# Kernel tuning notes

Measured on AMD Instinct MI355X. Metric: run time of the kernel, lower is better.

## Reference

```python
import jax, jax.numpy as jnp
import numpy as np

NLAT, NLON = 361, 720
LMAX = NLAT               # equiangular grid: lmax = nlat
MMAX = NLON // 2 + 1      # mmax = nlon//2 + 1
B, C = 1, 128


def _precompute_legpoly(mmax, lmax, t, csphase=True):
    """Associated Legendre vandermonde P_l^m(cos t), orthonormal, inverse=True
    (norm factor 1 for 'ortho'). Shape [mmax, lmax, nlat]. Setup-time numpy only."""
    x = np.cos(t)
    nmax = max(mmax, lmax)
    vdm = np.zeros((nmax, nmax, len(x)))
    vdm[0, 0] = np.sqrt(1.0 / (4.0 * np.pi))
    for l in range(1, nmax):
        vdm[l - 1, l] = np.sqrt(2 * l + 1) * x * vdm[l - 1, l - 1]
        vdm[l, l] = np.sqrt((2 * l + 1) * (1 + x) * (1 - x) / (2 * l)) * vdm[l - 1, l - 1]
    for l in range(2, nmax):
        for m in range(l - 1):
            a = np.sqrt((2 * l - 1) / (l - m) * (2 * l + 1) / (l + m))
            b = np.sqrt((l + m - 1) / (l - m) * (2 * l + 1) / (2 * l - 3) * (l - m - 1) / (l + m))
            vdm[m, l] = a * x * vdm[m, l - 1] - b * vdm[m, l - 2]
    vdm = vdm[:mmax, :lmax]
    if csphase:
        vdm[1::2] *= -1.0  # Condon-Shortley phase on odd m
    return vdm


def setup_inputs() -> dict:
    key = jax.random.key(0)
    # spherical harmonic coefficients as real view: [B, C, lmax, mmax, 2]
    x_real = jax.random.normal(key, (B, C, LMAX, MMAX, 2), dtype=jnp.float32)
    # equiangular (Clenshaw-Curtiss) colatitudes, t = flip(arccos(cos(pi*j/(n-1))))
    t = np.pi * np.arange(NLAT) / (NLAT - 1)
    pct = jnp.asarray(_precompute_legpoly(MMAX, LMAX, t), dtype=jnp.float32)  # [mmax, lmax, nlat]
    return {"x_real": x_real, "pct": pct}


def reference(x_real, pct):
    # single-device case: comm sizes == 1, all distributed transposes are identity
    # and nlatpad == nlonpad == 0.
    # per-m triangular Legendre contraction over l (torch einsum '...lmr,mlk->...kmr')
    xs = jnp.einsum('bclmr,mlk->bckmr', x_real, pct)        # [B, C, nlat, mmax, 2]
    xc = jax.lax.complex(xs[..., 0], xs[..., 1])            # [B, C, nlat, mmax]
    # inverse real FFT along longitude, norm='forward' (no 1/n scaling on inverse)
    out = jnp.fft.irfft(xc, n=NLON, axis=-1, norm='forward')  # [B, C, nlat, nlon]
    return out.astype(x_real.dtype)
```

## Files before the change

kernel.cpp:

```cpp
#include <hip/hip_runtime.h>
#include <cstddef>

#define CC   128
#define LDIM 361
#define MDIM 361
#define KDIM 361
#define NLON 720
#define LP   384
#define KP   384
#define KTP  384
#define MRP  736
#define NP   768
#define CK   (CC*KDIM)
#define CR   (2*CC)

typedef __attribute__((ext_vector_type(8))) short short8;
typedef __attribute__((ext_vector_type(4))) float floatx4;

__device__ __forceinline__ unsigned short f2bf(float f) {
    union { float f; unsigned u; } v; v.f = f;
    unsigned u = v.u;
    u += 0x7fffu + ((u >> 16) & 1u);
    return (unsigned short)(u >> 16);
}

__device__ __forceinline__ void async_copy16(const void* g, void* l) {
    __builtin_amdgcn_global_load_lds(
        (const __attribute__((address_space(1))) void*)g,
        (__attribute__((address_space(3))) void*)l, 16, 0, 0);
}

__device__ __forceinline__ int xcd_swz(int id, int P) {
    int x = id & 7, g = id >> 3;
    int q = P >> 3, r = P & 7;
    int start = (x < r) ? x * (q + 1) : r * (q + 1) + (x - r) * q;
    return start + g;
}

__global__ void sht_gen_T(unsigned short* __restrict__ Tp) {
    int idx = blockIdx.x * 256 + threadIdx.x;
    if (idx >= NP * MRP) return;
    int n = idx / MRP, mr = idx - n * MRP;
    float v = 0.f;
    if (n < NLON && mr < 2 * MDIM) {
        int m = mr >> 1, im = mr & 1;
        if (m == 0)            v = im ? 0.f : 1.f;
        else if (m == MDIM-1)  v = im ? 0.f : ((n & 1) ? -1.f : 1.f);
        else {
            int ph = (m * n) % NLON;
            float ang = (float)ph * (float)(3.14159265358979323846 / 360.0);
            v = im ? (-2.f * sinf(ang)) : (2.f * cosf(ang));
        }
    }
    Tp[idx] = f2bf(v);
}

__global__ __launch_bounds__(256)
void sht_prep_x(const float* __restrict__ x, unsigned short* __restrict__ xA) {
    __shared__ float tp[2][32 * 65 + 4];
    const int mt = blockIdx.x;
    const int lt = blockIdx.y;
    const int c  = blockIdx.z;
    const int t  = threadIdx.x;

    #pragma unroll
    for (int u = 0; u < 8; ++u) {
        int p  = t + 256 * u;
        int li = p >> 5, mi = p & 31;
        int l = lt * 64 + li, m = mt * 32 + mi;
        float2 v = make_float2(0.f, 0.f);
        if (l < LDIM && m < MDIM)
            v = *(const float2*)(x + ((size_t)(c * LDIM + l) * MDIM + m) * 2);
        tp[0][mi * 65 + li] = v.x;
        tp[1][mi * 65 + li] = v.y;
    }
    __syncthreads();

    #pragma unroll
    for (int u = 0; u < 2; ++u) {
        int s  = t + 256 * u;
        int mi = s >> 4, rr = (s >> 3) & 1, lo = (s & 7) * 8;
        int m = mt * 32 + mi;
        if (m >= MDIM) continue;
        const float* pl = &tp[rr][mi * 65];
        short8 h;
        #pragma unroll
        for (int e = 0; e < 8; ++e)
            h[e] = (short)f2bf(pl[lo + e]);
        *(short8*)(xA + ((size_t)m * CR + 2 * c + rr) * LP + lt * 64 + lo) = h;
    }
}

__global__ __launch_bounds__(256)
void sht_prep_pct(const float* __restrict__ pct, unsigned short* __restrict__ pctT) {
    __shared__ float tile[64][65];
    const int m  = blockIdx.y;
    const int bx = blockIdx.x;
    const int kt = bx % 6, lt = bx / 6;
    const int l0 = lt * 64, k0 = kt * 64;
    const int t  = threadIdx.x;

    const int ki = t & 63, lb = t >> 6;
    #pragma unroll
    for (int u = 0; u < 16; ++u) {
        int li = lb + 4 * u;
        int l = l0 + li, k = k0 + ki;
        float v = 0.f;
        if (l < LDIM && k < KDIM)
            v = pct[((size_t)m * LDIM + l) * KDIM + k];
        tile[li][ki] = v;
    }
    __syncthreads();

    #pragma unroll
    for (int u = 0; u < 2; ++u) {
        int s = t + 256 * u;
        int ko = s >> 3, lo = (s & 7) * 8;
        short8 h;
        #pragma unroll
        for (int e = 0; e < 8; ++e)
            h[e] = (short)f2bf(tile[lo + e][ko]);
        *(short8*)(pctT + ((size_t)m * KP + k0 + ko) * LP + l0 + lo) = h;
    }
}

__global__ __launch_bounds__(512)
void sht_stageA6(const unsigned short* __restrict__ pctT, const unsigned short* __restrict__ xA,
                 unsigned short* __restrict__ xsT) {
    __shared__ unsigned short As[3][128 * 32];
    __shared__ unsigned short Bs[3][384 * 32];

    const int p   = xcd_swz(blockIdx.x, 2 * MDIM);
    const int m   = p >> 1, ct = p & 1;
    const int c0  = ct * 128;
    const int t   = threadIdx.x;
    const int w   = t >> 6, L = t & 63;
    const int wr  = w & 1, wc = w >> 1;
    const int lane15 = L & 15, quad = L >> 4;
    const int arr = t >> 2, alq = (t & 3) ^ (arr & 3);

    const unsigned short* xAm = xA + (size_t)m * CR * LP;
    const unsigned short* pTm = pctT + (size_t)m * KP * LP;

    floatx4 acc[4][6] = {};

    auto stage = [&](int buf, int kb) {
        async_copy16(xAm + (size_t)(c0 + arr) * LP + kb + alq * 8,
                     &As[buf][(w * 64) * 8]);
        #pragma unroll
        for (int u = 0; u < 3; ++u) {
            int s = u * 512 + t;
            int rr = s >> 2, lq = (s & 3) ^ (rr & 3);
            async_copy16(pTm + (size_t)rr * LP + kb + lq * 8,
                         &Bs[buf][(u * 512 + w * 64) * 8]);
        }
    };

    const int NT = LP / 32;
    stage(0, 0);
    stage(1, 32);

    for (int it = 0; it < NT; ++it) {
        const int cb = it % 3;
        if (it + 1 < NT) { asm volatile("s_waitcnt vmcnt(4)" ::: "memory"); }
        else             { asm volatile("s_waitcnt vmcnt(0)" ::: "memory"); }
        __builtin_amdgcn_sched_barrier(0);
        __builtin_amdgcn_s_barrier();
        __builtin_amdgcn_sched_barrier(0);

        short8 af[4], bf[6];
        #pragma unroll
        for (int i = 0; i < 4; ++i) {
            int row = wr * 64 + i * 16 + lane15;
            af[i] = *(const short8*)&As[cb][(row * 4 + (quad ^ (row & 3))) * 8];
        }
        #pragma unroll
        for (int j = 0; j < 6; ++j) {
            int row = wc * 96 + j * 16 + lane15;
            bf[j] = *(const short8*)&Bs[cb][(row * 4 + (quad ^ (row & 3))) * 8];
        }
        __builtin_amdgcn_s_setprio(1);
        #pragma unroll
        for (int i = 0; i < 4; ++i)
            #pragma unroll
            for (int j = 0; j < 6; ++j)
                acc[i][j] = __builtin_amdgcn_mfma_f32_16x16x32_bf16(af[i], bf[j], acc[i][j], 0, 0, 0);
        __builtin_amdgcn_s_setprio(0);

        if (it + 2 < NT) stage((it + 2) % 3, (it + 2) * 32);
    }

    #pragma unroll
    for (int i = 0; i < 4; ++i) {
        #pragma unroll
        for (int j = 0; j < 6; ++j) {
            int k = wc * 96 + j * 16 + lane15;
            #pragma unroll
            for (int e = 0; e < 4; ++e) {
                int cr = c0 + wr * 64 + i * 16 + quad * 4 + e;
                xsT[((size_t)m * CR + cr) * KTP + k] = f2bf(acc[i][j][e]);
            }
        }
    }
}

__global__ __launch_bounds__(256)
void sht_xs_tr(const unsigned short* __restrict__ xsT, unsigned short* __restrict__ xs) {
    __shared__ unsigned tile32[64 * 65];
    const int c  = blockIdx.y;
    const int bx = blockIdx.x;
    const int mt = bx / 6, kt = bx % 6;
    const int m0 = mt * 64, k0 = kt * 64;
    const int t  = threadIdx.x;

    #pragma unroll
    for (int u = 0; u < 2; ++u) {
        int q  = t + 256 * u;
        int mi = q >> 3, ko8 = q & 7;
        int m  = m0 + mi;
        short8 a = {}, b = {};
        if (m < MDIM) {
            const unsigned short* base = xsT + ((size_t)m * CR + 2 * c) * KTP + k0 + ko8 * 8;
            a = *(const short8*)base;
            b = *(const short8*)(base + KTP);
        }
        #pragma unroll
        for (int e = 0; e < 8; ++e)
            tile32[(ko8 * 8 + e) * 65 + mi] =
                (unsigned)(unsigned short)a[e] | ((unsigned)(unsigned short)b[e] << 16);
    }
    __syncthreads();

    #pragma unroll
    for (int u = 0; u < 4; ++u) {
        int q  = t + 256 * u;
        int kk = q >> 4, mc = q & 15;
        int k  = k0 + kk;
        int mr0 = 2 * m0 + mc * 8;
        if (k >= KDIM || mr0 >= MRP) continue;
        unsigned w0 = tile32[kk * 65 + mc * 4 + 0];
        unsigned w1 = tile32[kk * 65 + mc * 4 + 1];
        unsigned w2 = tile32[kk * 65 + mc * 4 + 2];
        unsigned w3 = tile32[kk * 65 + mc * 4 + 3];
        unsigned* dst = (unsigned*)(xs + (size_t)(c * KDIM + k) * MRP + mr0);
        dst[0] = w0; dst[1] = w1; dst[2] = w2; dst[3] = w3;
    }
}

__global__ __launch_bounds__(512)
void sht_stageA2(const unsigned short* __restrict__ pctT, const unsigned short* __restrict__ xA,
                 unsigned short* __restrict__ xs) {
    __shared__ unsigned short As[128 * 32];
    __shared__ unsigned short Bs[384 * 32];

    const int p   = xcd_swz(blockIdx.x, 2 * MDIM);
    const int m   = p >> 1, ct = p & 1;
    const int c0  = ct * 128;
    const int t   = threadIdx.x;
    const int w   = t >> 6, L = t & 63;
    const int wr  = w & 1, wc = w >> 1;
    const int lane15 = L & 15, quad = L >> 4;
    const int arr = t >> 2, alq = t & 3;

    const unsigned short* xAm = xA + (size_t)m * CR * LP;
    const unsigned short* pTm = pctT + (size_t)m * KP * LP;

    floatx4 acc[4][6] = {};

    for (int kb = 0; kb < LP; kb += 32) {
        async_copy16(xAm + (size_t)(c0 + arr) * LP + kb + alq * 8,
                     As + (size_t)(w * 64) * 8);
        #pragma unroll
        for (int u = 0; u < 3; ++u) {
            int s = u * 512 + t;
            int rr = s >> 2, lq = s & 3;
            async_copy16(pTm + (size_t)rr * LP + kb + lq * 8,
                         Bs + (size_t)(u * 512 + w * 64) * 8);
        }
        __syncthreads();

        short8 af[4], bf[6];
        #pragma unroll
        for (int i = 0; i < 4; ++i)
            af[i] = *(const short8*)&As[((wr * 64 + i * 16 + lane15) * 4 + quad) * 8];
        #pragma unroll
        for (int j = 0; j < 6; ++j)
            bf[j] = *(const short8*)&Bs[((wc * 96 + j * 16 + lane15) * 4 + quad) * 8];
        #pragma unroll
        for (int i = 0; i < 4; ++i)
            #pragma unroll
            for (int j = 0; j < 6; ++j)
                acc[i][j] = __builtin_amdgcn_mfma_f32_16x16x32_bf16(af[i], bf[j], acc[i][j], 0, 0, 0);
        __syncthreads();
    }

    #pragma unroll
    for (int j = 0; j < 6; ++j) {
        int k = wc * 96 + j * 16 + lane15;
        if (k >= KDIM) continue;
        #pragma unroll
        for (int i = 0; i < 4; ++i) {
            #pragma unroll
            for (int eh = 0; eh < 2; ++eh) {
                int cr = c0 + wr * 64 + i * 16 + quad * 4 + eh * 2;
                int c  = cr >> 1;
                unsigned pack = (unsigned)f2bf(acc[i][j][eh * 2]) |
                                ((unsigned)f2bf(acc[i][j][eh * 2 + 1]) << 16);
                *(unsigned*)(xs + (size_t)(c * KDIM + k) * MRP + 2 * m) = pack;
            }
        }
    }
}

__global__ __launch_bounds__(256)
void sht_stageA(const float* __restrict__ pct, const unsigned short* __restrict__ xA,
                unsigned short* __restrict__ xs) {
    __shared__ unsigned short As[128 * 32];
    __shared__ unsigned short Bs[32 * 130];

    const int m   = blockIdx.y;
    const int ct  = blockIdx.x & 1;
    const int kt  = blockIdx.x >> 1;
    const int c0  = ct * 128;
    const int n0  = kt * 128;
    const int t   = threadIdx.x;
    const int w   = t >> 6, L = t & 63;
    const int wr  = w & 1, wc = w >> 1;
    const int lane15 = L & 15, quad = L >> 4;
    const int bl = t >> 3, bkq = t & 7;

    const unsigned short* xAm = xA + (size_t)m * CR * LP;
    const float* pctm = pct + (size_t)m * LDIM * KDIM;

    floatx4 acc[4][4] = {};

    for (int kb = 0; kb < LP; kb += 32) {
        #pragma unroll
        for (int i = 0; i < 2; ++i) {
            int s = w * 128 + i * 64 + L;
            int cr = s >> 2, lq = s & 3;
            async_copy16(xAm + (size_t)(c0 + cr) * LP + kb + lq * 8,
                         As + (size_t)(w * 128 + i * 64) * 8);
        }
        {
            int l = kb + bl;
            bool lok = (l < LDIM);
            const float* prow = pctm + (size_t)l * KDIM;
            #pragma unroll
            for (int u = 0; u < 4; ++u) {
                int kc = n0 + u * 32 + bkq * 4;
                float f0 = (lok && kc + 0 < KDIM) ? prow[kc + 0] : 0.f;
                float f1 = (lok && kc + 1 < KDIM) ? prow[kc + 1] : 0.f;
                float f2 = (lok && kc + 2 < KDIM) ? prow[kc + 2] : 0.f;
                float f3 = (lok && kc + 3 < KDIM) ? prow[kc + 3] : 0.f;
                unsigned* bp = (unsigned*)&Bs[bl * 130 + u * 32 + bkq * 4];
                bp[0] = (unsigned)f2bf(f0) | ((unsigned)f2bf(f1) << 16);
                bp[1] = (unsigned)f2bf(f2) | ((unsigned)f2bf(f3) << 16);
            }
        }
        __syncthreads();

        short8 af[4];
        #pragma unroll
        for (int i = 0; i < 4; ++i) {
            int row = wr * 64 + i * 16 + lane15;
            af[i] = *(const short8*)&As[(row * 4 + quad) * 8];
        }
        #pragma unroll
        for (int jf = 0; jf < 4; ++jf) {
            int col = wc * 64 + jf * 16 + lane15;
            short8 bf;
            #pragma unroll
            for (int j = 0; j < 8; ++j)
                bf[j] = (short)Bs[(quad * 8 + j) * 130 + col];
            #pragma unroll
            for (int i = 0; i < 4; ++i)
                acc[i][jf] = __builtin_amdgcn_mfma_f32_16x16x32_bf16(af[i], bf, acc[i][jf], 0, 0, 0);
        }
        __syncthreads();
    }

    #pragma unroll
    for (int i = 0; i < 4; ++i) {
        #pragma unroll
        for (int jf = 0; jf < 4; ++jf) {
            int k = n0 + wc * 64 + jf * 16 + lane15;
            if (k >= KDIM) continue;
            #pragma unroll
            for (int eh = 0; eh < 2; ++eh) {
                int cr = c0 + wr * 64 + i * 16 + quad * 4 + eh * 2;
                int c  = cr >> 1;
                unsigned pack = (unsigned)f2bf(acc[i][jf][eh * 2]) |
                                ((unsigned)f2bf(acc[i][jf][eh * 2 + 1]) << 16);
                *(unsigned*)(xs + (size_t)(c * KDIM + k) * MRP + 2 * m) = pack;
            }
        }
    }
}

__global__ __launch_bounds__(512)
void sht_stageB5(const unsigned short* __restrict__ xs, const unsigned short* __restrict__ Tp,
                 float* __restrict__ out) {
    __shared__ unsigned short As[3][128 * 32];
    __shared__ unsigned short Bs[3][384 * 32];

    const int p   = xcd_swz(blockIdx.x, 2 * MDIM);
    const int ckt = p >> 1, nt = p & 1;
    const int ck0 = ckt * 128, n0 = nt * 384;
    const int t   = threadIdx.x;
    const int w   = t >> 6, L = t & 63;
    const int wr  = w & 1, wc = w >> 1;
    const int lane15 = L & 15, quad = L >> 4;
    const int arr = t >> 2, alq = (t & 3) ^ (arr & 3);

    floatx4 acc[4][6] = {};

    auto stage = [&](int buf, int kb) {
        async_copy16(xs + (size_t)(ck0 + arr) * MRP + kb + alq * 8,
                     &As[buf][(w * 64) * 8]);
        #pragma unroll
        for (int u = 0; u < 3; ++u) {
            int s = u * 512 + t;
            int rr = s >> 2, lq = (s & 3) ^ (rr & 3);
            async_copy16(Tp + (size_t)(n0 + rr) * MRP + kb + lq * 8,
                         &Bs[buf][(u * 512 + w * 64) * 8]);
        }
    };

    const int NT = MRP / 32;
    stage(0, 0);
    stage(1, 32);

    for (int it = 0; it < NT; ++it) {
        const int cb = it % 3;
        if (it + 1 < NT) { asm volatile("s_waitcnt vmcnt(4)" ::: "memory"); }
        else             { asm volatile("s_waitcnt vmcnt(0)" ::: "memory"); }
        __builtin_amdgcn_sched_barrier(0);
        __builtin_amdgcn_s_barrier();
        __builtin_amdgcn_sched_barrier(0);

        short8 af[4], bf[6];
        #pragma unroll
        for (int i = 0; i < 4; ++i) {
            int row = wr * 64 + i * 16 + lane15;
            af[i] = *(const short8*)&As[cb][(row * 4 + (quad ^ (row & 3))) * 8];
        }
        #pragma unroll
        for (int j = 0; j < 6; ++j) {
            int row = wc * 96 + j * 16 + lane15;
            bf[j] = *(const short8*)&Bs[cb][(row * 4 + (quad ^ (row & 3))) * 8];
        }
        __builtin_amdgcn_s_setprio(1);
        #pragma unroll
        for (int i = 0; i < 4; ++i)
            #pragma unroll
            for (int j = 0; j < 6; ++j)
                acc[i][j] = __builtin_amdgcn_mfma_f32_16x16x32_bf16(af[i], bf[j], acc[i][j], 0, 0, 0);
        __builtin_amdgcn_s_setprio(0);

        if (it + 2 < NT) stage((it + 2) % 3, (it + 2) * 32);
    }

    #pragma unroll
    for (int i = 0; i < 4; ++i) {
        int ckr = ck0 + wr * 64 + i * 16 + quad * 4;
        #pragma unroll
        for (int j = 0; j < 6; ++j) {
            int jj = n0 + wc * 96 + j * 16 + lane15;
            if (jj >= NLON) continue;
            #pragma unroll
            for (int e = 0; e < 4; ++e)
                out[(size_t)(ckr + e) * NLON + jj] = acc[i][j][e];
        }
    }
}

extern "C" void kernel_launch(void* const* d_in, const int* in_sizes, int n_in,
                              void* d_out, int out_size, void* d_ws, size_t ws_size,
                              hipStream_t stream) {
    const float* x   = (const float*)d_in[0];
    const float* pct = (const float*)d_in[1];
    float* out = (float*)d_out;

    unsigned short* xs = (unsigned short*)d_ws;
    unsigned short* Tp = xs + (size_t)CK * MRP;
    unsigned short* xA = (unsigned short*)d_out;

    const size_t base_shorts = (size_t)CK * MRP + (size_t)NP * MRP;
    const size_t pctT_shorts = (size_t)MDIM * KP * LP;
    const size_t xsT_shorts  = (size_t)MDIM * CR * KTP;
    const bool fast1 = ws_size >= (base_shorts + pctT_shorts) * sizeof(unsigned short);
    const bool fast2 = ws_size >= (base_shorts + pctT_shorts + xsT_shorts) * sizeof(unsigned short);

    sht_gen_T<<<(NP * MRP + 255) / 256, 256, 0, stream>>>(Tp);
    sht_prep_x<<<dim3(12, 6, 128), 256, 0, stream>>>(x, xA);
    if (fast2) {
        unsigned short* pctT = Tp + (size_t)NP * MRP;
        unsigned short* xsT  = pctT + pctT_shorts;
        sht_prep_pct<<<dim3(36, MDIM), 256, 0, stream>>>(pct, pctT);
        sht_stageA6<<<dim3(2 * MDIM), 512, 0, stream>>>(pctT, xA, xsT);
        sht_xs_tr<<<dim3(36, 128), 256, 0, stream>>>(xsT, xs);
    } else if (fast1) {
        unsigned short* pctT = Tp + (size_t)NP * MRP;
        sht_prep_pct<<<dim3(36, MDIM), 256, 0, stream>>>(pct, pctT);
        sht_stageA2<<<dim3(2 * MDIM), 512, 0, stream>>>(pctT, xA, xs);
    } else {
        sht_stageA<<<dim3(6, MDIM), 256, 0, stream>>>(pct, xA, xs);
    }
    sht_stageB5<<<dim3(2 * MDIM), 512, 0, stream>>>(xs, Tp, out);
}
```

Before: 582.8 us.

## Shrink GEMM tiles to 64-row blocks with double-buffered LDS pipeline

Measured after the change: 690.0 us. +18.4%, slower.

```diff
diff --git a/kernel.cpp b/kernel.cpp
--- a/kernel.cpp
+++ b/kernel.cpp
@@ -13,6 +13,7 @@
 #define NP   768
 #define CK   (CC*KDIM)
 #define CR   (2*CC)
+#define CKT  722
 
 typedef __attribute__((ext_vector_type(8))) short short8;
 typedef __attribute__((ext_vector_type(4))) float floatx4;
@@ -124,18 +125,18 @@
     }
 }
 
-__global__ __launch_bounds__(512)
-void sht_stageA6(const unsigned short* __restrict__ pctT, const unsigned short* __restrict__ xA,
+__global__ __launch_bounds__(256)
+void sht_stageA7(const unsigned short* __restrict__ pctT, const unsigned short* __restrict__ xA,
                  unsigned short* __restrict__ xsT) {
-    __shared__ unsigned short As[3][128 * 32];
-    __shared__ unsigned short Bs[3][384 * 32];
-
-    const int p   = xcd_swz(blockIdx.x, 2 * MDIM);
-    const int m   = p >> 1, ct = p & 1;
-    const int c0  = ct * 128;
+    __shared__ unsigned short As[2][64 * 32];
+    __shared__ unsigned short Bs[2][384 * 32];
+
+    const int p   = xcd_swz(blockIdx.x, 4 * MDIM);
+    const int m   = p >> 2, ct = p & 3;
+    const int c0  = ct * 64;
     const int t   = threadIdx.x;
     const int w   = t >> 6, L = t & 63;
-    const int wr  = w & 1, wc = w >> 1;
+    const int wc  = w;
     const int lane15 = L & 15, quad = L >> 4;
     const int arr = t >> 2, alq = (t & 3) ^ (arr & 3);
 
@@ -148,22 +149,25 @@
         async_copy16(xAm + (size_t)(c0 + arr) * LP + kb + alq * 8,
                      &As[buf][(w * 64) * 8]);
         #pragma unroll
-        for (int u = 0; u < 3; ++u) {
-            int s = u * 512 + t;
+        for (int u = 0; u < 6; ++u) {
+            int s = u * 256 + t;
             int rr = s >> 2, lq = (s & 3) ^ (rr & 3);
             async_copy16(pTm + (size_t)rr * LP + kb + lq * 8,
-                         &Bs[buf][(u * 512 + w * 64) * 8]);
+                         &Bs[buf][(u * 256 + w * 64) * 8]);
         }
     };
 
     const int NT = LP / 32;
     stage(0, 0);
-    stage(1, 32);
 
     for (int it = 0; it < NT; ++it) {
-        const int cb = it % 3;
-        if (it + 1 < NT) { asm volatile("s_waitcnt vmcnt(4)" ::: "memory"); }
-        else             { asm volatile("s_waitcnt vmcnt(0)" ::: "memory"); }
+        const int cur = it & 1;
+        if (it + 1 < NT) {
+            stage(cur ^ 1, (it + 1) * 32);
+            asm volatile("s_waitcnt vmcnt(7)" ::: "memory");
+        } else {
+            asm volatile("s_waitcnt vmcnt(0)" ::: "memory");
+        }
         __builtin_amdgcn_sched_barrier(0);
         __builtin_amdgcn_s_barrier();
         __builtin_amdgcn_sched_barrier(0);
@@ -171,14 +175,19 @@
         short8 af[4], bf[6];
         #pragma unroll
         for (int i = 0; i < 4; ++i) {
-            int row = wr * 64 + i * 16 + lane15;
-            af[i] = *(const short8*)&As[cb][(row * 4 + (quad ^ (row & 3))) * 8];
+            int row = i * 16 + lane15;
+            af[i] = *(const short8*)&As[cur][(row * 4 + (quad ^ (row & 3))) * 8];
         }
         #pragma unroll
         for (int j = 0; j < 6; ++j) {
             int row = wc * 96 + j * 16 + lane15;
-            bf[j] = *(const short8*)&Bs[cb][(row * 4 + (quad ^ (row & 3))) * 8];
-        }
+            bf[j] = *(const short8*)&Bs[cur][(row * 4 + (quad ^ (row & 3))) * 8];
+        }
+        asm volatile("s_waitcnt lgkmcnt(0)" ::: "memory");
+        __builtin_amdgcn_sched_barrier(0);
+        __builtin_amdgcn_s_barrier();
+        __builtin_amdgcn_sched_barrier(0);
+
         __builtin_amdgcn_s_setprio(1);
         #pragma unroll
         for (int i = 0; i < 4; ++i)
@@ -186,8 +195,6 @@
             for (int j = 0; j < 6; ++j)
                 acc[i][j] = __builtin_amdgcn_mfma_f32_16x16x32_bf16(af[i], bf[j], acc[i][j], 0, 0, 0);
         __builtin_amdgcn_s_setprio(0);
-
-        if (it + 2 < NT) stage((it + 2) % 3, (it + 2) * 32);
     }
 
     #pragma unroll
@@ -197,7 +204,7 @@
             int k = wc * 96 + j * 16 + lane15;
             #pragma unroll
             for (int e = 0; e < 4; ++e) {
-                int cr = c0 + wr * 64 + i * 16 + quad * 4 + e;
+                int cr = c0 + i * 16 + quad * 4 + e;
                 xsT[((size_t)m * CR + cr) * KTP + k] = f2bf(acc[i][j][e]);
             }
         }
@@ -398,18 +405,18 @@
     }
 }
 
-__global__ __launch_bounds__(512)
-void sht_stageB5(const unsigned short* __restrict__ xs, const unsigned short* __restrict__ Tp,
+__global__ __launch_bounds__(256)
+void sht_stageB6(const unsigned short* __restrict__ xs, const unsigned short* __restrict__ Tp,
                  float* __restrict__ out) {
-    __shared__ unsigned short As[3][128 * 32];
-    __shared__ unsigned short Bs[3][384 * 32];
-
-    const int p   = xcd_swz(blockIdx.x, 2 * MDIM);
+    __shared__ unsigned short As[2][64 * 32];
+    __shared__ unsigned short Bs[2][384 * 32];
+
+    const int p   = xcd_swz(blockIdx.x, 2 * CKT);
     const int ckt = p >> 1, nt = p & 1;
-    const int ck0 = ckt * 128, n0 = nt * 384;
+    const int ck0 = ckt * 64, n0 = nt * 384;
     const int t   = threadIdx.x;
     const int w   = t >> 6, L = t & 63;
-    const int wr  = w & 1, wc = w >> 1;
+    const int wc  = w;
     const int lane15 = L & 15, quad = L >> 4;
     const int arr = t >> 2, alq = (t & 3) ^ (arr & 3);
 
@@ -419,22 +426,25 @@
         async_copy16(xs + (size_t)(ck0 + arr) * MRP + kb + alq * 8,
                      &As[buf][(w * 64) * 8]);
         #pragma unroll
-        for (int u = 0; u < 3; ++u) {
-            int s = u * 512 + t;
+        for (int u = 0; u < 6; ++u) {
+            int s = u * 256 + t;
             int rr = s >> 2, lq = (s & 3) ^ (rr & 3);
             async_copy16(Tp + (size_t)(n0 + rr) * MRP + kb + lq * 8,
-                         &Bs[buf][(u * 512 + w * 64) * 8]);
+                         &Bs[buf][(u * 256 + w * 64) * 8]);
         }
     };
 
     const int NT = MRP / 32;
     stage(0, 0);
-    stage(1, 32);
 
     for (int it = 0; it < NT; ++it) {
-        const int cb = it % 3;
-        if (it + 1 < NT) { asm volatile("s_waitcnt vmcnt(4)" ::: "memory"); }
-        else             { asm volatile("s_waitcnt vmcnt(0)" ::: "memory"); }
+        const int cur = it & 1;
+        if (it + 1 < NT) {
+            stage(cur ^ 1, (it + 1) * 32);
+            asm volatile("s_waitcnt vmcnt(7)" ::: "memory");
+        } else {
+            asm volatile("s_waitcnt vmcnt(0)" ::: "memory");
+        }
         __builtin_amdgcn_sched_barrier(0);
         __builtin_amdgcn_s_barrier();
         __builtin_amdgcn_sched_barrier(0);
@@ -442,14 +452,19 @@
         short8 af[4], bf[6];
         #pragma unroll
         for (int i = 0; i < 4; ++i) {
-            int row = wr * 64 + i * 16 + lane15;
-            af[i] = *(const short8*)&As[cb][(row * 4 + (quad ^ (row & 3))) * 8];
+            int row = i * 16 + lane15;
+            af[i] = *(const short8*)&As[cur][(row * 4 + (quad ^ (row & 3))) * 8];
         }
         #pragma unroll
         for (int j = 0; j < 6; ++j) {
             int row = wc * 96 + j * 16 + lane15;
-            bf[j] = *(const short8*)&Bs[cb][(row * 4 + (quad ^ (row & 3))) * 8];
-        }
+            bf[j] = *(const short8*)&Bs[cur][(row * 4 + (quad ^ (row & 3))) * 8];
+        }
+        asm volatile("s_waitcnt lgkmcnt(0)" ::: "memory");
+        __builtin_amdgcn_sched_barrier(0);
+        __builtin_amdgcn_s_barrier();
+        __builtin_amdgcn_sched_barrier(0);
+
         __builtin_amdgcn_s_setprio(1);
         #pragma unroll
         for (int i = 0; i < 4; ++i)
@@ -457,13 +472,11 @@
             for (int j = 0; j < 6; ++j)
                 acc[i][j] = __builtin_amdgcn_mfma_f32_16x16x32_bf16(af[i], bf[j], acc[i][j], 0, 0, 0);
         __builtin_amdgcn_s_setprio(0);
-
-        if (it + 2 < NT) stage((it + 2) % 3, (it + 2) * 32);
     }
 
     #pragma unroll
     for (int i = 0; i < 4; ++i) {
-        int ckr = ck0 + wr * 64 + i * 16 + quad * 4;
+        int ckr = ck0 + i * 16 + quad * 4;
         #pragma unroll
         for (int j = 0; j < 6; ++j) {
             int jj = n0 + wc * 96 + j * 16 + lane15;
@@ -498,7 +511,7 @@
         unsigned short* pctT = Tp + (size_t)NP * MRP;
         unsigned short* xsT  = pctT + pctT_shorts;
         sht_prep_pct<<<dim3(36, MDIM), 256, 0, stream>>>(pct, pctT);
-        sht_stageA6<<<dim3(2 * MDIM), 512, 0, stream>>>(pctT, xA, xsT);
+        sht_stageA7<<<dim3(4 * MDIM), 256, 0, stream>>>(pctT, xA, xsT);
         sht_xs_tr<<<dim3(36, 128), 256, 0, stream>>>(xsT, xs);
     } else if (fast1) {
         unsigned short* pctT = Tp + (size_t)NP * MRP;
@@ -507,5 +520,5 @@
     } else {
         sht_stageA<<<dim3(6, MDIM), 256, 0, stream>>>(pct, xA, xs);
     }
-    sht_stageB5<<<dim3(2 * MDIM), 512, 0, stream>>>(xs, Tp, out);
-}
+    sht_stageB6<<<dim3(2 * CKT), 256, 0, stream>>>(xs, Tp, out);
+}
```
